# Optimization experiments

Hardware: AMD Instinct MI355X
Metric: run time of the kernel (lower is better)

## Reference

```python
import jax, jax.numpy as jnp
import numpy as np

N_NODES = 100000


def gcn_conv(x, edge_index, W, b):
    # GCNConv with add_self_loops=True, normalize=True (symmetric norm):
    # out = D^{-1/2} (A + I) D^{-1/2} (x @ W) + b
    n = x.shape[0]
    h = x @ W  # transform first (PyG applies lin before propagate)
    src, dst = edge_index[0], edge_index[1]
    ones = jnp.ones(src.shape[0], dtype=h.dtype)
    # degree with self-loops: in-degree + 1
    deg = jax.ops.segment_sum(ones, dst, num_segments=n) + 1.0
    dinv = jax.lax.rsqrt(deg)  # deg >= 1, always finite
    # per-edge normalized messages, scatter-add to dst
    msg = h[src] * (dinv[src] * dinv[dst])[:, None]
    agg = jax.ops.segment_sum(msg, dst, num_segments=n)
    # self-loop contribution: norm = dinv[i]^2
    agg = agg + h * (dinv * dinv)[:, None]
    return agg + b


def setup_inputs() -> dict:
    key = jax.random.key(0)
    ks = jax.random.split(key, 8)
    x = jax.random.normal(ks[0], (N_NODES, 256), dtype=jnp.float32)
    edge_index = jax.random.randint(ks[1], (2, 3200000), 0, N_NODES, dtype=jnp.int32)
    W1 = jax.random.normal(ks[2], (256, 32), dtype=jnp.float32) * (1.0 / np.sqrt(256))
    b1 = jnp.zeros((32,), dtype=jnp.float32)
    Wm = jax.random.normal(ks[3], (32, 16), dtype=jnp.float32) * (1.0 / np.sqrt(32))
    bm = jnp.zeros((16,), dtype=jnp.float32)
    Wv = jax.random.normal(ks[4], (32, 16), dtype=jnp.float32) * (1.0 / np.sqrt(32))
    bv = jnp.zeros((16,), dtype=jnp.float32)
    return {"x": x, "edge_index": edge_index, "W1": W1, "b1": b1,
            "Wm": Wm, "bm": bm, "Wv": Wv, "bv": bv}


def reference(x, edge_index, W1, b1, Wm, bm, Wv, bv):
    h = jax.nn.relu(gcn_conv(x, edge_index, W1, b1))
    mu = gcn_conv(h, edge_index, Wm, bm)
    sigma = gcn_conv(h, edge_index, Wv, bv)
    return (mu, sigma)
```

## Files before the change

### kernel.cpp

```cpp
#include <hip/hip_runtime.h>
#include <hip/hip_fp16.h>

#define NNODES 100000
#define NEDGES 3200000
#define F_IN   256
#define F_HID  32
#define F_OUT  16

#define NB   196
#define NPB  512
#define NCHUNK 256
#define CHUNK  12500

#define GR 64
#define GRID1 ((NNODES + GR - 1) / GR)


__global__ void k_init(int* __restrict__ bhist) {
    if (threadIdx.x < NB) bhist[threadIdx.x] = 0;
}

__global__ __launch_bounds__(256) void k_bhist(const int* __restrict__ dst,
                                               int* __restrict__ bhist) {
    __shared__ int lh[NB];
    int t = threadIdx.x;
    for (int i = t; i < NB; i += 256) lh[i] = 0;
    __syncthreads();
    for (int i = blockIdx.x * 256 + t; i < NEDGES; i += gridDim.x * 256)
        atomicAdd(&lh[dst[i] >> 9], 1);
    __syncthreads();
    for (int i = t; i < NB; i += 256)
        if (lh[i]) atomicAdd(&bhist[i], lh[i]);
}

__global__ __launch_bounds__(256) void k_bscan(const int* __restrict__ bhist,
                                               int* __restrict__ bbase,
                                               int* __restrict__ bcur) {
    __shared__ int s[256];
    int t = threadIdx.x;
    int my = (t < NB) ? bhist[t] : 0;
    s[t] = my;
    __syncthreads();
    #pragma unroll
    for (int d = 1; d < 256; d <<= 1) {
        int v = (t >= d) ? s[t - d] : 0;
        __syncthreads();
        s[t] += v;
        __syncthreads();
    }
    if (t < NB) {
        int ex = s[t] - my;
        bbase[t] = ex;
        bcur[t]  = ex;
        if (t == NB - 1) bbase[NB] = s[t];
    }
}

__global__ __launch_bounds__(256) void k_phaseA(
        const int* __restrict__ src, const int* __restrict__ dst,
        int* __restrict__ bcur, unsigned int* __restrict__ rec) {
    __shared__ int lh[NB];
    __shared__ int lcur[NB];
    int t = threadIdx.x;
    int e0 = blockIdx.x * CHUNK;
    for (int i = t; i < NB; i += 256) lh[i] = 0;
    __syncthreads();
    for (int i = t; i < CHUNK; i += 256)
        atomicAdd(&lh[dst[e0 + i] >> 9], 1);
    __syncthreads();
    for (int i = t; i < NB; i += 256)
        lcur[i] = lh[i] ? atomicAdd(&bcur[i], lh[i]) : 0;
    __syncthreads();
    for (int i = t; i < CHUNK; i += 256) {
        int s = src[e0 + i], d = dst[e0 + i];
        int b = d >> 9;
        int pos = atomicAdd(&lcur[b], 1);
        rec[pos] = ((unsigned)s << 9) | (unsigned)(d & 511);
    }
}

__global__ __launch_bounds__(1024) void k_phaseB(
        const unsigned int* __restrict__ rec, const int* __restrict__ bbase,
        int* __restrict__ rowptr, float* __restrict__ dinv, int* __restrict__ csr) {
    __shared__ int lh[NPB];
    __shared__ int lsc[NPB];
    int t = threadIdx.x, b = blockIdx.x;
    int lo = bbase[b], hi = bbase[b + 1];
    for (int i = t; i < NPB; i += 1024) lh[i] = 0;
    __syncthreads();
    for (int i = lo + t; i < hi; i += 1024)
        atomicAdd(&lh[rec[i] & 511], 1);
    __syncthreads();
    if (t < NPB) lsc[t] = lh[t];
    __syncthreads();
    #pragma unroll
    for (int d = 1; d < NPB; d <<= 1) {
        int v = 0;
        if (t < NPB && t >= d) v = lsc[t - d];
        __syncthreads();
        if (t < NPB) lsc[t] += v;
        __syncthreads();
    }
    if (t < NPB) {
        int node = b * NPB + t;
        if (node < NNODES) {
            int ex = lsc[t] - lh[t];
            rowptr[node] = lo + ex;
            dinv[node] = rsqrtf((float)lh[t] + 1.0f);
        }
    }
    if (b == NB - 1 && t == 0) rowptr[NNODES] = NEDGES;
    __syncthreads();
    if (t < NPB) lsc[t] -= lh[t];
    __syncthreads();
    for (int i = lo + t; i < hi; i += 1024) {
        unsigned r = rec[i];
        int dl = r & 511;
        int p = atomicAdd(&lsc[dl], 1);
        csr[lo + p] = (int)(r >> 9);
    }
}


__global__ __launch_bounds__(256) void k_gemm1(
        const float* __restrict__ x, const float* __restrict__ W1,
        const float* __restrict__ dinv, __half2* __restrict__ g1) {
    __shared__ float Wl[F_IN * F_HID];
    int t = threadIdx.x;
    for (int i = t; i < (F_IN * F_HID) / 4; i += 256)
        ((float4*)Wl)[i] = ((const float4*)W1)[i];
    __syncthreads();

    int fg = (t & 7) * 4;
    int rg = (t >> 3) * 2;
    int row0 = blockIdx.x * GR + rg;

    const float* xr0 = x + (size_t)min(row0 + 0, NNODES - 1) * F_IN;
    const float* xr1 = x + (size_t)min(row0 + 1, NNODES - 1) * F_IN;

    float acc[2][4] = {};
    #pragma unroll 4
    for (int k = 0; k < F_IN; k += 4) {
        float4 xv0 = *(const float4*)&xr0[k];
        float4 xv1 = *(const float4*)&xr1[k];
        #pragma unroll
        for (int kk = 0; kk < 4; ++kk) {
            float4 wv = *(const float4*)&Wl[(k + kk) * F_HID + fg];
            float xs0 = (&xv0.x)[kk], xs1 = (&xv1.x)[kk];
            acc[0][0] = fmaf(xs0, wv.x, acc[0][0]);
            acc[0][1] = fmaf(xs0, wv.y, acc[0][1]);
            acc[0][2] = fmaf(xs0, wv.z, acc[0][2]);
            acc[0][3] = fmaf(xs0, wv.w, acc[0][3]);
            acc[1][0] = fmaf(xs1, wv.x, acc[1][0]);
            acc[1][1] = fmaf(xs1, wv.y, acc[1][1]);
            acc[1][2] = fmaf(xs1, wv.z, acc[1][2]);
            acc[1][3] = fmaf(xs1, wv.w, acc[1][3]);
        }
    }
    #pragma unroll
    for (int j = 0; j < 2; ++j) {
        int row = row0 + j;
        if (row < NNODES) {
            float dv = dinv[row];
            __half2 ha = __floats2half2_rn(acc[j][0] * dv, acc[j][1] * dv);
            __half2 hb = __floats2half2_rn(acc[j][2] * dv, acc[j][3] * dv);
            g1[(size_t)row * 16 + (fg >> 1)]     = ha;
            g1[(size_t)row * 16 + (fg >> 1) + 1] = hb;
        }
    }
}


__global__ __launch_bounds__(256) void k_gather_l1(
        const int* __restrict__ rowptr, const int* __restrict__ csr,
        const float* __restrict__ dinv, const __half2* __restrict__ g,
        const float* __restrict__ b1, const float* __restrict__ Wm,
        const float* __restrict__ Wv, __half2* __restrict__ g2) {
    __shared__ float Wcat[F_HID * 32];
    __shared__ float hrow[16][F_HID + 2];
    int tx = threadIdx.x;
    for (int idx = tx; idx < F_HID * 32; idx += 256) {
        int k = idx >> 5, j = idx & 31;
        Wcat[idx] = (j < F_OUT) ? Wm[k * F_OUT + j] : Wv[k * F_OUT + (j - F_OUT)];
    }
    int f2 = tx & 15;
    int lr = tx >> 4;
    int node = blockIdx.x * 16 + lr;
    int start = rowptr[node], end = rowptr[node + 1];
    float2 acc = __half22float2(g[(size_t)node * 16 + f2]);
    int j = start;
    for (; j + 4 <= end; j += 4) {
        int s0 = csr[j], s1 = csr[j + 1], s2 = csr[j + 2], s3 = csr[j + 3];
        float2 a0 = __half22float2(g[(size_t)s0 * 16 + f2]);
        float2 a1 = __half22float2(g[(size_t)s1 * 16 + f2]);
        float2 a2 = __half22float2(g[(size_t)s2 * 16 + f2]);
        float2 a3 = __half22float2(g[(size_t)s3 * 16 + f2]);
        acc.x += (a0.x + a1.x) + (a2.x + a3.x);
        acc.y += (a0.y + a1.y) + (a2.y + a3.y);
    }
    for (; j < end; ++j) {
        float2 a = __half22float2(g[(size_t)csr[j] * 16 + f2]);
        acc.x += a.x; acc.y += a.y;
    }
    float dv = dinv[node];
    float h0 = dv * acc.x + b1[2 * f2];
    float h1 = dv * acc.y + b1[2 * f2 + 1];
    hrow[lr][2 * f2]     = h0 > 0.f ? h0 : 0.f;
    hrow[lr][2 * f2 + 1] = h1 > 0.f ? h1 : 0.f;
    __syncthreads();
    float o0 = 0.f, o1 = 0.f;
    #pragma unroll
    for (int k = 0; k < F_HID; ++k) {
        float hv = hrow[lr][k];
        o0 = fmaf(hv, Wcat[k * 32 + 2 * f2], o0);
        o1 = fmaf(hv, Wcat[k * 32 + 2 * f2 + 1], o1);
    }
    g2[(size_t)node * 16 + f2] = __floats2half2_rn(o0 * dv, o1 * dv);
}


__global__ __launch_bounds__(256) void k_gather_out(
        const int* __restrict__ rowptr, const int* __restrict__ csr,
        const float* __restrict__ dinv, const __half2* __restrict__ g,
        const float* __restrict__ bm, const float* __restrict__ bv,
        float* __restrict__ out) {
    int tx = threadIdx.x;
    int f2 = tx & 15;
    int node = blockIdx.x * 16 + (tx >> 4);
    int start = rowptr[node], end = rowptr[node + 1];
    float2 acc = __half22float2(g[(size_t)node * 16 + f2]);
    int j = start;
    for (; j + 4 <= end; j += 4) {
        int s0 = csr[j], s1 = csr[j + 1], s2 = csr[j + 2], s3 = csr[j + 3];
        float2 a0 = __half22float2(g[(size_t)s0 * 16 + f2]);
        float2 a1 = __half22float2(g[(size_t)s1 * 16 + f2]);
        float2 a2 = __half22float2(g[(size_t)s2 * 16 + f2]);
        float2 a3 = __half22float2(g[(size_t)s3 * 16 + f2]);
        acc.x += (a0.x + a1.x) + (a2.x + a3.x);
        acc.y += (a0.y + a1.y) + (a2.y + a3.y);
    }
    for (; j < end; ++j) {
        float2 a = __half22float2(g[(size_t)csr[j] * 16 + f2]);
        acc.x += a.x; acc.y += a.y;
    }
    float dv = dinv[node];
    int f = 2 * f2;
    if (f < F_OUT) {
        float2 o = { dv * acc.x + bm[f], dv * acc.y + bm[f + 1] };
        *(float2*)&out[(size_t)node * F_OUT + f] = o;
    } else {
        float2 o = { dv * acc.x + bv[f - F_OUT], dv * acc.y + bv[f - F_OUT + 1] };
        *(float2*)&out[(size_t)NNODES * F_OUT + (size_t)node * F_OUT + (f - F_OUT)] = o;
    }
}


extern "C" void kernel_launch(void* const* d_in, const int* in_sizes, int n_in,
                              void* d_out, int out_size, void* d_ws, size_t ws_size,
                              hipStream_t stream) {
    const float* x   = (const float*)d_in[0];
    const int*   ei  = (const int*)  d_in[1];
    const float* W1  = (const float*)d_in[2];
    const float* b1  = (const float*)d_in[3];
    const float* Wm  = (const float*)d_in[4];
    const float* bm  = (const float*)d_in[5];
    const float* Wv  = (const float*)d_in[6];
    const float* bv  = (const float*)d_in[7];
    float* out = (float*)d_out;

    const int* src = ei;
    const int* dst = ei + NEDGES;

    char* ws = (char*)d_ws;
    float*        dinv   = (float*)ws;        ws += 100352 * 4;
    int*          bhist  = (int*)ws;          ws += 256 * 4;
    int*          bbase  = (int*)ws;          ws += 256 * 4;
    int*          bcur   = (int*)ws;          ws += 256 * 4;
    int*          rowptr = (int*)ws;          ws += 100352 * 4;
    int*          csr    = (int*)ws;          ws += (size_t)NEDGES * 4;
    unsigned int* rec    = (unsigned int*)ws; ws += (size_t)NEDGES * 4;
    __half2*      g2     = (__half2*)ws;

    __half2* g1 = (__half2*)rec;

    k_init  <<<1, 256, 0, stream>>>(bhist);
    k_bhist <<<256, 256, 0, stream>>>(dst, bhist);
    k_bscan <<<1, 256, 0, stream>>>(bhist, bbase, bcur);
    k_phaseA<<<NCHUNK, 256, 0, stream>>>(src, dst, bcur, rec);
    k_phaseB<<<NB, 1024, 0, stream>>>(rec, bbase, rowptr, dinv, csr);

    k_gemm1<<<GRID1, 256, 0, stream>>>(x, W1, dinv, g1);

    k_gather_l1<<<NNODES / 16, 256, 0, stream>>>(rowptr, csr, dinv, g1, b1, Wm, Wv, g2);

    k_gather_out<<<NNODES / 16, 256, 0, stream>>>(rowptr, csr, dinv, g2, bm, bv, out);
}
```

Before: 394.1 us.

## Compute first-layer GEMM with fp16 MFMA instructions instead of scalar FMAs

Rewrites the x@W1 kernel so each wave computes a 16x32 tile using two mfma_f32_16x16x32_f16 ops per K chunk, converting x and W1 to fp16 in registers. Results are staged through shared memory, scaled by dinv, and written as packed half2 rows. This targets the scalar FMA throughput and the shared-memory weight loads of the old kernel, but it rounds inputs to fp16, which loses precision, and each thread now loads W1 directly from global memory.

```diff
diff --git a/kernel.cpp b/kernel.cpp
--- a/kernel.cpp
+++ b/kernel.cpp
@@ -12,8 +12,11 @@
 #define NCHUNK 256
 #define CHUNK  12500
 
-#define GR 64
-#define GRID1 ((NNODES + GR - 1) / GR)
+#define GRID1 ((NNODES + 63) / 64)
+
+typedef _Float16 half_t;
+typedef half_t half8 __attribute__((ext_vector_type(8)));
+typedef float f32x4 __attribute__((ext_vector_type(4)));
 
 
 __global__ void k_init(int* __restrict__ bhist) {
@@ -125,48 +128,65 @@
 __global__ __launch_bounds__(256) void k_gemm1(
         const float* __restrict__ x, const float* __restrict__ W1,
         const float* __restrict__ dinv, __half2* __restrict__ g1) {
-    __shared__ float Wl[F_IN * F_HID];
+    __shared__ float sbuf[4][16 * 33];
     int t = threadIdx.x;
-    for (int i = t; i < (F_IN * F_HID) / 4; i += 256)
-        ((float4*)Wl)[i] = ((const float4*)W1)[i];
-    __syncthreads();
-
-    int fg = (t & 7) * 4;
-    int rg = (t >> 3) * 2;
-    int row0 = blockIdx.x * GR + rg;
-
-    const float* xr0 = x + (size_t)min(row0 + 0, NNODES - 1) * F_IN;
-    const float* xr1 = x + (size_t)min(row0 + 1, NNODES - 1) * F_IN;
-
-    float acc[2][4] = {};
-    #pragma unroll 4
-    for (int k = 0; k < F_IN; k += 4) {
-        float4 xv0 = *(const float4*)&xr0[k];
-        float4 xv1 = *(const float4*)&xr1[k];
+    int wave = t >> 6, lane = t & 63;
+    int m = lane & 15, q = lane >> 4;
+
+    int row0 = blockIdx.x * 64 + wave * 16;
+
+    half8 B[2][8];
+    #pragma unroll
+    for (int kc = 0; kc < 8; ++kc) {
         #pragma unroll
-        for (int kk = 0; kk < 4; ++kk) {
-            float4 wv = *(const float4*)&Wl[(k + kk) * F_HID + fg];
-            float xs0 = (&xv0.x)[kk], xs1 = (&xv1.x)[kk];
-            acc[0][0] = fmaf(xs0, wv.x, acc[0][0]);
-            acc[0][1] = fmaf(xs0, wv.y, acc[0][1]);
-            acc[0][2] = fmaf(xs0, wv.z, acc[0][2]);
-            acc[0][3] = fmaf(xs0, wv.w, acc[0][3]);
-            acc[1][0] = fmaf(xs1, wv.x, acc[1][0]);
-            acc[1][1] = fmaf(xs1, wv.y, acc[1][1]);
-            acc[1][2] = fmaf(xs1, wv.z, acc[1][2]);
-            acc[1][3] = fmaf(xs1, wv.w, acc[1][3]);
+        for (int j = 0; j < 8; ++j) {
+            int k = kc * 32 + q * 8 + j;
+            B[0][kc][j] = (half_t)W1[k * F_HID + m];
+            B[1][kc][j] = (half_t)W1[k * F_HID + 16 + m];
         }
     }
-    #pragma unroll
-    for (int j = 0; j < 2; ++j) {
-        int row = row0 + j;
-        if (row < NNODES) {
-            float dv = dinv[row];
-            __half2 ha = __floats2half2_rn(acc[j][0] * dv, acc[j][1] * dv);
-            __half2 hb = __floats2half2_rn(acc[j][2] * dv, acc[j][3] * dv);
-            g1[(size_t)row * 16 + (fg >> 1)]     = ha;
-            g1[(size_t)row * 16 + (fg >> 1) + 1] = hb;
-        }
+
+    int row = row0 + m; if (row >= NNODES) row = NNODES - 1;
+    const float* xr = x + (size_t)row * F_IN;
+
+    f32x4 acc0 = {0.f, 0.f, 0.f, 0.f};
+    f32x4 acc1 = {0.f, 0.f, 0.f, 0.f};
+    #pragma unroll
+    for (int kc = 0; kc < 8; ++kc) {
+        int k = kc * 32 + q * 8;
+        float4 xa = *(const float4*)&xr[k];
+        float4 xb = *(const float4*)&xr[k + 4];
+        half8 A;
+        A[0] = (half_t)xa.x; A[1] = (half_t)xa.y;
+        A[2] = (half_t)xa.z; A[3] = (half_t)xa.w;
+        A[4] = (half_t)xb.x; A[5] = (half_t)xb.y;
+        A[6] = (half_t)xb.z; A[7] = (half_t)xb.w;
+        acc0 = __builtin_amdgcn_mfma_f32_16x16x32_f16(A, B[0][kc], acc0, 0, 0, 0);
+        acc1 = __builtin_amdgcn_mfma_f32_16x16x32_f16(A, B[1][kc], acc1, 0, 0, 0);
+    }
+
+    #pragma unroll
+    for (int r = 0; r < 4; ++r) {
+        int rl = q * 4 + r;
+        int grow = row0 + rl; if (grow >= NNODES) grow = NNODES - 1;
+        float dv = dinv[grow];
+        sbuf[wave][rl * 33 + m]      = acc0[r] * dv;
+        sbuf[wave][rl * 33 + 16 + m] = acc1[r] * dv;
+    }
+    __syncthreads();
+
+    int rl  = (t >> 2) & 15;
+    int w2  = t >> 6;
+    int c0  = (t & 3) * 8;
+    int grow = blockIdx.x * 64 + w2 * 16 + rl;
+    if (grow < NNODES) {
+        const float* sp = &sbuf[w2][rl * 33 + c0];
+        __half2 h0 = __floats2half2_rn(sp[0], sp[1]);
+        __half2 h1 = __floats2half2_rn(sp[2], sp[3]);
+        __half2 h2 = __floats2half2_rn(sp[4], sp[5]);
+        __half2 h3 = __floats2half2_rn(sp[6], sp[7]);
+        __half2* gp = &g1[(size_t)grow * 16 + (c0 >> 1)];
+        gp[0] = h0; gp[1] = h1; gp[2] = h2; gp[3] = h3;
     }
 }
 
```

New measurement: 382.2 us. -3.0%, faster.
